# Performance work log

Hardware: AMD Instinct MI355X
Metric: run time of the kernel (lower is better)

## Reference

```python
import jax, jax.numpy as jnp
import numpy as np
from jax import lax

H = W = 16   # grid_size
C = 64       # d_model
NH = 4       # attention heads
DH = C // NH
L = 2        # transformer layers
FF = 2048    # torch TransformerEncoderLayer default dim_feedforward
B = 8192
FEAT = 55


def _feats(pi, pj, gi, gj, wall):
    # pi,pj,gi,gj: scalar int32; wall: [H,W] float32
    f = jnp.float32
    ain = 2.0 * pi.astype(f) / (H - 1) - 1.0
    ajn = 2.0 * pj.astype(f) / (W - 1) - 1.0
    gin = 2.0 * gi.astype(f) / (H - 1) - 1.0
    gjn = 2.0 * gj.astype(f) / (W - 1) - 1.0
    dxg = gjn - ajn
    dyg = gin - ain
    dg = jnp.sqrt(dxg * dxg + dyg * dyg + 1e-8)
    goal = jnp.stack([ain, ajn, gin, gjn, dxg, dyg, dg, dyg / dg, dxg / dg])
    # first (up to) 3 wall locations in row-major order
    flat = wall.reshape(-1)
    idx = jnp.arange(H * W, dtype=jnp.int32)
    masked = jnp.where(flat == 1, idx, H * W)
    top3 = -lax.top_k(-masked, 3)[0]            # 3 smallest flat indices
    is_valid = top3 < H * W
    valid = is_valid.astype(f)
    safe = jnp.where(is_valid, top3, 0)
    win = 2.0 * (safe // W).astype(f) / (H - 1) - 1.0   # [3]
    wjn = 2.0 * (safe % W).astype(f) / (W - 1) - 1.0

    def rel(rin, rjn):
        dx = wjn - rjn
        dy = win - rin
        d = jnp.sqrt(dx * dx + dy * dy + 1e-8)
        return jnp.stack([win, wjn, dx, dy, d, dy / d, dx / d], axis=1)  # [3,7]

    aw = (rel(ain, ajn) * valid[:, None]).reshape(21)
    gw = (rel(gin, gjn) * valid[:, None]).reshape(21)
    up = jnp.where(pi > 0, wall[jnp.clip(pi - 1, 0, H - 1), pj], 1.0)
    dn = jnp.where(pi < H - 1, wall[jnp.clip(pi + 1, 0, H - 1), pj], 1.0)
    lf = jnp.where(pj > 0, wall[pi, jnp.clip(pj - 1, 0, W - 1)], 1.0)
    rt = jnp.where(pj < W - 1, wall[pi, jnp.clip(pj + 1, 0, W - 1)], 1.0)
    neigh = jnp.stack([up, dn, lf, rt])
    return jnp.concatenate([goal, aw, gw, neigh])  # [55]


def _ln(x, g, b):
    m = x.mean(-1, keepdims=True)
    v = ((x - m) ** 2).mean(-1, keepdims=True)
    return (x - m) / jnp.sqrt(v + 1e-5) * g + b


def _mha(x, wqkv, bqkv, wo, bo):
    # x: [B,T,C]
    qkv = x @ wqkv.T + bqkv               # [B,T,3C]
    q, k, v = jnp.split(qkv, 3, axis=-1)
    hds = lambda t: t.reshape(t.shape[0], t.shape[1], NH, DH).transpose(0, 2, 1, 3)
    q, k, v = hds(q), hds(k), hds(v)
    a = jax.nn.softmax(jnp.einsum('bhqd,bhkd->bhqk', q, k) / np.sqrt(DH).astype(np.float32), axis=-1)
    o = jnp.einsum('bhqk,bhkd->bhqd', a, v).transpose(0, 2, 1, 3).reshape(x.shape)
    return o @ wo.T + bo


def _forward(ai, aj, gi, gj, walls,
             mlp_w1, mlp_b1, mlp_w2, mlp_b2,
             in_proj_w, in_proj_b, out_w, out_b,
             ln1_g, ln1_b, ln2_g, ln2_b,
             ffn_w1, ffn_b1, ffn_w2, ffn_b2):
    wf = walls.astype(jnp.float32)
    # 5 positions per obs: current + 4 hypothetical moves (stay in place if off-grid)
    moves = jnp.array([[0, 0], [-1, 0], [1, 0], [0, -1], [0, 1]], dtype=jnp.int32)
    ni = ai[:, None] + moves[None, :, 0]
    nj = aj[:, None] + moves[None, :, 1]
    inb = (ni >= 0) & (ni < H) & (nj >= 0) & (nj < W)
    pi = jnp.where(inb, ni, ai[:, None])   # [B,5]
    pj = jnp.where(inb, nj, aj[:, None])
    per_obs = jax.vmap(_feats, in_axes=(0, 0, None, None, None))
    feats = jax.vmap(per_obs, in_axes=(0, 0, 0, 0, 0))(pi, pj, gi, gj, wf)  # [B,5,55]
    # feat_mlp: Linear -> GELU(exact) -> Linear
    tok = jax.nn.gelu(feats @ mlp_w1.T + mlp_b1, approximate=False) @ mlp_w2.T + mlp_b2  # [B,5,C]
    x = tok
    for l in range(L):
        x = _ln(x + _mha(x, in_proj_w[l], in_proj_b[l], out_w[l], out_b[l]), ln1_g[l], ln1_b[l])
        hdn = jax.nn.relu(x @ ffn_w1[l].T + ffn_b1[l]) @ ffn_w2[l].T + ffn_b2[l]
        x = _ln(x + hdn, ln2_g[l], ln2_b[l])
    return x  # [B,5,C]


def setup_inputs() -> dict:
    key = jax.random.key(0)
    ks = jax.random.split(key, 24)
    s = 0.02
    inp = {
        'ai': jax.random.randint(ks[0], (B,), 0, H, dtype=jnp.int32),
        'aj': jax.random.randint(ks[1], (B,), 0, W, dtype=jnp.int32),
        'gi': jax.random.randint(ks[2], (B,), 0, H, dtype=jnp.int32),
        'gj': jax.random.randint(ks[3], (B,), 0, W, dtype=jnp.int32),
        'walls': jax.random.randint(ks[4], (B, H, W), 0, 2, dtype=jnp.int32),
        'mlp_w1': jax.random.normal(ks[5], (128, FEAT)) * s,
        'mlp_b1': jnp.zeros((128,)),
        'mlp_w2': jax.random.normal(ks[6], (C, 128)) * s,
        'mlp_b2': jnp.zeros((C,)),
        'in_proj_w': jax.random.normal(ks[7], (L, 3 * C, C)) * s,
        'in_proj_b': jnp.zeros((L, 3 * C)),
        'out_w': jax.random.normal(ks[8], (L, C, C)) * s,
        'out_b': jnp.zeros((L, C)),
        'ln1_g': jnp.ones((L, C)),
        'ln1_b': jnp.zeros((L, C)),
        'ln2_g': jnp.ones((L, C)),
        'ln2_b': jnp.zeros((L, C)),
        'ffn_w1': jax.random.normal(ks[9], (L, FF, C)) * s,
        'ffn_b1': jnp.zeros((L, FF)),
        'ffn_w2': jax.random.normal(ks[10], (L, C, FF)) * s,
        'ffn_b2': jnp.zeros((L, C)),
    }
    return inp


def reference(ai, aj, gi, gj, walls,
              mlp_w1, mlp_b1, mlp_w2, mlp_b2,
              in_proj_w, in_proj_b, out_w, out_b,
              ln1_g, ln1_b, ln2_g, ln2_b,
              ffn_w1, ffn_b1, ffn_w2, ffn_b2):
    return _forward(ai, aj, gi, gj, walls,
                    mlp_w1, mlp_b1, mlp_w2, mlp_b2,
                    in_proj_w, in_proj_b, out_w, out_b,
                    ln1_g, ln1_b, ln2_g, ln2_b,
                    ffn_w1, ffn_b1, ffn_w2, ffn_b2)
```

## Files before the change

### kernel.cpp

```cpp
#include <hip/hip_runtime.h>
#include <math.h>

#define NT 256

typedef __attribute__((ext_vector_type(4))) float  f32x4;
typedef __attribute__((ext_vector_type(8))) short  bf16x8;
typedef __attribute__((ext_vector_type(4))) short  bf16x4;

static __device__ __forceinline__ short f2bf(float f) {
    unsigned u = __builtin_bit_cast(unsigned, f);
    unsigned r = (u + 0x7fffu + ((u >> 16) & 1u)) >> 16;
    return (short)r;
}

static __device__ __forceinline__ unsigned pk2(float a, float b) {
    unsigned ua = __builtin_bit_cast(unsigned, a);
    unsigned ub = __builtin_bit_cast(unsigned, b);
    ua = (ua + 0x7fffu + ((ua >> 16) & 1u)) >> 16;
    ub = (ub + 0x7fffu + ((ub >> 16) & 1u)) & 0xffff0000u;
    return ua | ub;
}
static __device__ __forceinline__ bf16x4 pk_bf16(f32x4 d) {
    uint2 t;
    t.x = pk2(d[0], d[1]);
    t.y = pk2(d[2], d[3]);
    return __builtin_bit_cast(bf16x4, t);
}
static __device__ __forceinline__ bf16x8 pk_bf16x8(f32x4 a, f32x4 b) {
    uint4 t;
    t.x = pk2(a[0], a[1]);
    t.y = pk2(a[2], a[3]);
    t.z = pk2(b[0], b[1]);
    t.w = pk2(b[2], b[3]);
    return __builtin_bit_cast(bf16x8, t);
}
static __device__ __forceinline__ bf16x4 lo4(bf16x8 v) {
    return __builtin_shufflevector(v, v, 0, 1, 2, 3);
}
static __device__ __forceinline__ bf16x4 hi4(bf16x8 v) {
    return __builtin_shufflevector(v, v, 4, 5, 6, 7);
}

#define MFMA16x32(a, b, c) __builtin_amdgcn_mfma_f32_16x16x32_bf16(a, b, c, 0, 0, 0)

#if __has_builtin(__builtin_amdgcn_mfma_f32_16x16x16bf16_1k)
static __device__ __forceinline__ f32x4 mfma16x16(bf16x4 a, bf16x4 b, f32x4 c) {
    return __builtin_amdgcn_mfma_f32_16x16x16bf16_1k(a, b, c, 0, 0, 0);
}
#elif __has_builtin(__builtin_amdgcn_mfma_f32_16x16x16_bf16)
static __device__ __forceinline__ f32x4 mfma16x16(bf16x4 a, bf16x4 b, f32x4 c) {
    return __builtin_amdgcn_mfma_f32_16x16x16_bf16(a, b, c, 0, 0, 0);
}
#else
static __device__ __forceinline__ f32x4 mfma16x16(bf16x4 a, bf16x4 b, f32x4 c) {
    f32x4 d;
    asm("v_mfma_f32_16x16x16_bf16 %0, %1, %2, %3" : "=v"(d) : "v"(a), "v"(b), "v"(c));
    return d;
}
#endif

#define WS_FPK  0
#define WS_QKV  524288
#define WS_WO   548864
#define WS_BASE 557056
#define WS_MW1  557056
#define WS_MW2  565248
#define WS_TOTAL 573440

__global__ __launch_bounds__(NT) void k_cvtw(
    const float* __restrict__ ffn_w1, const float* __restrict__ ffn_w2,
    const float* __restrict__ in_proj_w, const float* __restrict__ out_w,
    const float* __restrict__ mlp_w1, const float* __restrict__ mlp_w2,
    int do_mlp,
    unsigned short* __restrict__ ws)
{
    int i = blockIdx.x * NT + threadIdx.x;
    if (i < 524288) {
        int l = i >> 18;
        int w = i & 262143;
        int c = w >> 13;
        int ww = w & 8191;
        int region = ww >> 11;
        int q = ww & 2047;
        int lane = q >> 3, j = q & 7;
        int hc = lane >> 6, lg = (lane >> 4) & 3, lr = lane & 15;
        const float* W1 = ffn_w1 + l * 131072;
        const float* W2 = ffn_w2 + l * 131072;
        float v;
        if (region == 0)
            v = W1[(c * 64 + hc * 16 + lr) * 64 + lg * 8 + j];
        else if (region == 1)
            v = W1[(c * 64 + hc * 16 + lr) * 64 + 32 + lg * 8 + j];
        else {
            int nf = ((region - 2) << 1) + (j >> 2);
            int r = j & 3;
            v = W2[(nf * 16 + lr) * 2048 + c * 64 + hc * 16 + lg * 4 + r];
        }
        ws[WS_FPK + i] = (unsigned short)f2bf(v);
    }
    if (i < 24576) ws[WS_QKV + i] = (unsigned short)f2bf(in_proj_w[i]);
    if (i < 8192)  ws[WS_WO + i]  = (unsigned short)f2bf(out_w[i]);
    if (do_mlp && i < 8192) {
        int row = i >> 6, col = i & 63;
        ws[WS_MW1 + i] = (col < 55) ? (unsigned short)f2bf(mlp_w1[row * 55 + col]) : 0;
        ws[WS_MW2 + i] = (unsigned short)f2bf(mlp_w2[i]);
    }
}

#define FB 16
__global__ __launch_bounds__(320) void k_feat2(
    const int* __restrict__ ai, const int* __restrict__ aj,
    const int* __restrict__ gi, const int* __restrict__ gj,
    const int* __restrict__ walls,
    const unsigned short* __restrict__ w1p,
    const float* __restrict__ b1,
    const unsigned short* __restrict__ w2p,
    const float* __restrict__ b2,
    float* __restrict__ x)
{
    const int tid = threadIdx.x;
    const int ob0 = blockIdx.x * FB;
    __shared__ unsigned char wl[FB * 256];
    __shared__ short fe[80][72];
    __shared__ int t3s[FB][3];

    for (int i = tid; i < FB * 256; i += 320)
        wl[i] = (unsigned char)walls[ob0 * 256 + i];
    __syncthreads();

    const int lane = tid & 63;
    const int wid  = tid >> 6;

    if (wid < 4) {
        #pragma unroll
        for (int q = 0; q < 4; ++q) {
            const int o = wid * 4 + q;
            const unsigned char* wp = wl + o * 256 + lane * 4;
            int m = (wp[0] ? 1 : 0) | (wp[1] ? 2 : 0) | (wp[2] ? 4 : 0) | (wp[3] ? 8 : 0);
            unsigned long long bm[4];
            bm[0] = __ballot(m & 1); bm[1] = __ballot(m & 2);
            bm[2] = __ballot(m & 4); bm[3] = __ballot(m & 8);
            int res[3];
            #pragma unroll
            for (int c = 0; c < 3; ++c) {
                int best = 1 << 30, bj = -1;
                #pragma unroll
                for (int j = 0; j < 4; ++j)
                    if (bm[j]) {
                        int cand = 4 * (int)__builtin_ctzll(bm[j]) + j;
                        if (cand < best) { best = cand; bj = j; }
                    }
                res[c] = (bj >= 0) ? best : 256;
                if (bj >= 0) bm[bj] &= bm[bj] - 1;
            }
            if (lane == 0) {
                t3s[o][0] = res[0]; t3s[o][1] = res[1]; t3s[o][2] = res[2];
            }
        }
    }
    __syncthreads();

    if (tid < 80) {
        const int o = tid / 5, tq = tid % 5;
        const int gob = ob0 + o;
        const unsigned char* wp = wl + o * 256;
        const int mi[5] = {0, -1, 1, 0, 0};
        const int mj[5] = {0, 0, 0, -1, 1};
        const int a_i = ai[gob], a_j = aj[gob];
        int ni = a_i + mi[tq], nj = a_j + mj[tq];
        bool inb = (ni >= 0 && ni < 16 && nj >= 0 && nj < 16);
        int pi = inb ? ni : a_i;
        int pj = inb ? nj : a_j;

        float f[64];
        #pragma unroll
        for (int d = 55; d < 64; ++d) f[d] = 0.f;

        const float ain = 2.f * (float)pi / 15.f - 1.f;
        const float ajn = 2.f * (float)pj / 15.f - 1.f;
        const float gin = 2.f * (float)gi[gob] / 15.f - 1.f;
        const float gjn = 2.f * (float)gj[gob] / 15.f - 1.f;
        const float dxg = gjn - ajn, dyg = gin - ain;
        const float dg = sqrtf(dxg * dxg + dyg * dyg + 1e-8f);
        f[0] = ain; f[1] = ajn; f[2] = gin; f[3] = gjn;
        f[4] = dxg; f[5] = dyg; f[6] = dg; f[7] = dyg / dg; f[8] = dxg / dg;

        #pragma unroll
        for (int w = 0; w < 3; ++w) {
            int idx = t3s[o][w];
            float vm = (idx < 256) ? 1.f : 0.f;
            int safe = (idx < 256) ? idx : 0;
            float win = 2.f * (float)(safe >> 4) / 15.f - 1.f;
            float wjn = 2.f * (float)(safe & 15) / 15.f - 1.f;
            {
                float dx = wjn - ajn, dy = win - ain;
                float d = sqrtf(dx * dx + dy * dy + 1e-8f);
                f[9 + w * 7 + 0] = win * vm; f[9 + w * 7 + 1] = wjn * vm;
                f[9 + w * 7 + 2] = dx * vm;  f[9 + w * 7 + 3] = dy * vm;
                f[9 + w * 7 + 4] = d * vm;
                f[9 + w * 7 + 5] = (dy / d) * vm; f[9 + w * 7 + 6] = (dx / d) * vm;
            }
            {
                float dx = wjn - gjn, dy = win - gin;
                float d = sqrtf(dx * dx + dy * dy + 1e-8f);
                f[30 + w * 7 + 0] = win * vm; f[30 + w * 7 + 1] = wjn * vm;
                f[30 + w * 7 + 2] = dx * vm;  f[30 + w * 7 + 3] = dy * vm;
                f[30 + w * 7 + 4] = d * vm;
                f[30 + w * 7 + 5] = (dy / d) * vm; f[30 + w * 7 + 6] = (dx / d) * vm;
            }
        }
        f[51] = (pi > 0)  ? (float)wp[(pi - 1) * 16 + pj] : 1.f;
        f[52] = (pi < 15) ? (float)wp[(pi + 1) * 16 + pj] : 1.f;
        f[53] = (pj > 0)  ? (float)wp[pi * 16 + (pj - 1)] : 1.f;
        f[54] = (pj < 15) ? (float)wp[pi * 16 + (pj + 1)] : 1.f;

        unsigned* dst = (unsigned*)&fe[tid][0];
        #pragma unroll
        for (int d = 0; d < 32; ++d)
            dst[d] = pk2(f[2 * d], f[2 * d + 1]);
    }
    __syncthreads();

    const int lr = lane & 15;
    const int lg = lane >> 4;
    const int t0 = wid * 16;

    bf16x8 bf0 = *(const bf16x8*)&fe[t0 + lr][lg * 8];
    bf16x8 bf1 = *(const bf16x8*)&fe[t0 + lr][32 + lg * 8];

    f32x4 acc[4] = {};
    #pragma unroll
    for (int hc = 0; hc < 8; ++hc) {
        bf16x8 a0 = *(const bf16x8*)(w1p + (hc * 16 + lr) * 64 + lg * 8);
        bf16x8 a1 = *(const bf16x8*)(w1p + (hc * 16 + lr) * 64 + 32 + lg * 8);
        f32x4 d = {0.f, 0.f, 0.f, 0.f};
        d = MFMA16x32(a0, bf0, d);
        d = MFMA16x32(a1, bf1, d);
        f32x4 b1v = *(const f32x4*)(b1 + hc * 16 + lg * 4);
        bf16x4 h;
        #pragma unroll
        for (int r = 0; r < 4; ++r) {
            float s = d[r] + b1v[r];
            h[r] = f2bf(0.5f * s * (1.f + erff(s * 0.70710678118654752f)));
        }
        #pragma unroll
        for (int nf = 0; nf < 4; ++nf) {
            bf16x4 bw = *(const bf16x4*)(w2p + (nf * 16 + lr) * 128 + hc * 16 + lg * 4);
            acc[nf] = mfma16x16(h, bw, acc[nf]);
        }
    }

    const int gt0 = blockIdx.x * 80 + t0;
    #pragma unroll
    for (int r = 0; r < 4; ++r) {
        const int row = (gt0 + lg * 4 + r) * 64;
        #pragma unroll
        for (int nf = 0; nf < 4; ++nf)
            x[row + nf * 16 + lr] = acc[nf][r] + b2[nf * 16 + lr];
    }
}

__global__ __launch_bounds__(NT) void k_feat(
    const int* __restrict__ ai, const int* __restrict__ aj,
    const int* __restrict__ gi, const int* __restrict__ gj,
    const int* __restrict__ walls,
    const float* __restrict__ w1, const float* __restrict__ b1,
    const float* __restrict__ w2, const float* __restrict__ b2,
    float* __restrict__ xout)
{
    const int b = blockIdx.x;
    const int tid = threadIdx.x;
    __shared__ float wallf[256];
    __shared__ unsigned long long wmask[4];
    __shared__ int   t3[3];
    __shared__ float feats[5][55];
    __shared__ float h1[5][128];

    int wv = walls[b * 256 + tid];
    wallf[tid] = (float)wv;
    unsigned long long bm = __ballot(wv == 1);
    if ((tid & 63) == 0) wmask[tid >> 6] = bm;
    __syncthreads();

    if (tid == 0) {
        int c = 0;
        for (int w = 0; w < 4 && c < 3; ++w) {
            unsigned long long mm = wmask[w];
            while (mm && c < 3) {
                t3[c++] = w * 64 + __builtin_ctzll(mm);
                mm &= mm - 1;
            }
        }
        for (; c < 3; ++c) t3[c] = 256;
    }
    __syncthreads();

    if (tid < 5) {
        const int mi[5] = {0, -1, 1, 0, 0};
        const int mj[5] = {0, 0, 0, -1, 1};
        const int a_i = ai[b], a_j = aj[b];
        int ni = a_i + mi[tid], nj = a_j + mj[tid];
        bool inb = (ni >= 0 && ni < 16 && nj >= 0 && nj < 16);
        int pi = inb ? ni : a_i;
        int pj = inb ? nj : a_j;

        const float ain = 2.f * (float)pi / 15.f - 1.f;
        const float ajn = 2.f * (float)pj / 15.f - 1.f;
        const float gin = 2.f * (float)gi[b] / 15.f - 1.f;
        const float gjn = 2.f * (float)gj[b] / 15.f - 1.f;
        const float dxg = gjn - ajn, dyg = gin - ain;
        const float dg = sqrtf(dxg * dxg + dyg * dyg + 1e-8f);

        float* f = feats[tid];
        f[0] = ain; f[1] = ajn; f[2] = gin; f[3] = gjn;
        f[4] = dxg; f[5] = dyg; f[6] = dg; f[7] = dyg / dg; f[8] = dxg / dg;

        for (int w = 0; w < 3; ++w) {
            int idx = t3[w];
            float vm = (idx < 256) ? 1.f : 0.f;
            int safe = (idx < 256) ? idx : 0;
            float win = 2.f * (float)(safe >> 4) / 15.f - 1.f;
            float wjn = 2.f * (float)(safe & 15) / 15.f - 1.f;
            {
                float dx = wjn - ajn, dy = win - ain;
                float d = sqrtf(dx * dx + dy * dy + 1e-8f);
                float* o = f + 9 + w * 7;
                o[0] = win * vm; o[1] = wjn * vm; o[2] = dx * vm; o[3] = dy * vm;
                o[4] = d * vm;  o[5] = (dy / d) * vm; o[6] = (dx / d) * vm;
            }
            {
                float dx = wjn - gjn, dy = win - gin;
                float d = sqrtf(dx * dx + dy * dy + 1e-8f);
                float* o = f + 30 + w * 7;
                o[0] = win * vm; o[1] = wjn * vm; o[2] = dx * vm; o[3] = dy * vm;
                o[4] = d * vm;  o[5] = (dy / d) * vm; o[6] = (dx / d) * vm;
            }
        }
        f[51] = (pi > 0)  ? wallf[(pi - 1) * 16 + pj] : 1.f;
        f[52] = (pi < 15) ? wallf[(pi + 1) * 16 + pj] : 1.f;
        f[53] = (pj > 0)  ? wallf[pi * 16 + (pj - 1)] : 1.f;
        f[54] = (pj < 15) ? wallf[pi * 16 + (pj + 1)] : 1.f;
    }
    __syncthreads();

    for (int i = tid; i < 640; i += NT) {
        int p = i >> 7, j = i & 127;
        float s = b1[j];
        const float* wr = w1 + j * 55;
        const float* fp = feats[p];
        #pragma unroll
        for (int k = 0; k < 55; ++k) s += fp[k] * wr[k];
        h1[p][j] = 0.5f * s * (1.f + erff(s * 0.70710678118654752f));
    }
    __syncthreads();

    for (int i = tid; i < 320; i += NT) {
        int p = i >> 6, j = i & 63;
        float s = b2[j];
        const float* wr = w2 + j * 128;
        #pragma unroll
        for (int k = 0; k < 128; ++k) s += h1[p][k] * wr[k];
        xout[b * 320 + i] = s;
    }
}

__global__ __launch_bounds__(256, 2) void k_att3(
    const float* __restrict__ x, float* __restrict__ xo,
    const unsigned short* __restrict__ wqkv,
    const float* __restrict__ bqkv,
    const unsigned short* __restrict__ wo,
    const float* __restrict__ bo,
    const float* __restrict__ g1, const float* __restrict__ be1)
{
    const int tid  = threadIdx.x;
    const int lane = tid & 63;
    const int wid  = tid >> 6;
    const int lr = lane & 15;
    const int lg = lane >> 4;
    const int o0 = blockIdx.x * 16;

    __shared__ unsigned short o_sh[5][16][68];
    __shared__ float          y_sh[5][16][68];

    bf16x8 bx[5][2];
    #pragma unroll
    for (int tq = 0; tq < 5; ++tq)
        #pragma unroll
        for (int kf = 0; kf < 2; ++kf) {
            const float* p = x + ((o0 + lr) * 5 + tq) * 64 + kf * 32 + lg * 8;
            f32x4 aa = *(const f32x4*)(p);
            f32x4 bb = *(const f32x4*)(p + 4);
            bx[tq][kf] = pk_bf16x8(aa, bb);
        }

    {
        const int h = wid;
        bf16x8 aq[2], ak[2], av[2];
        #pragma unroll
        for (int kf = 0; kf < 2; ++kf) {
            aq[kf] = *(const bf16x8*)(wqkv + (h * 16 + lr) * 64 + kf * 32 + lg * 8);
            ak[kf] = *(const bf16x8*)(wqkv + (64 + h * 16 + lr) * 64 + kf * 32 + lg * 8);
            av[kf] = *(const bf16x8*)(wqkv + (128 + h * 16 + lr) * 64 + kf * 32 + lg * 8);
        }
        f32x4 bq = *(const f32x4*)(bqkv + h * 16 + lg * 4);
        f32x4 bk = *(const f32x4*)(bqkv + 64 + h * 16 + lg * 4);
        f32x4 bv = *(const f32x4*)(bqkv + 128 + h * 16 + lg * 4);

        f32x4 qf[5], kf_[5], vf[5];
        #pragma unroll
        for (int t = 0; t < 5; ++t) {
            f32x4 d = {0.f, 0.f, 0.f, 0.f};
            d = MFMA16x32(aq[0], bx[t][0], d);
            d = MFMA16x32(aq[1], bx[t][1], d);
            qf[t] = d + bq;
            f32x4 e = {0.f, 0.f, 0.f, 0.f};
            e = MFMA16x32(ak[0], bx[t][0], e);
            e = MFMA16x32(ak[1], bx[t][1], e);
            kf_[t] = e + bk;
            f32x4 g = {0.f, 0.f, 0.f, 0.f};
            g = MFMA16x32(av[0], bx[t][0], g);
            g = MFMA16x32(av[1], bx[t][1], g);
            vf[t] = g + bv;
        }

        float p_[5][5];
        #pragma unroll
        for (int tq = 0; tq < 5; ++tq)
            #pragma unroll
            for (int tk = 0; tk < 5; ++tk) {
                float s = qf[tq][0] * kf_[tk][0] + qf[tq][1] * kf_[tk][1]
                        + qf[tq][2] * kf_[tk][2] + qf[tq][3] * kf_[tk][3];
                s += __shfl_xor(s, 16);
                s += __shfl_xor(s, 32);
                p_[tq][tk] = s * 0.25f;
            }
        #pragma unroll
        for (int tq = 0; tq < 5; ++tq) {
            float m = p_[tq][0];
            #pragma unroll
            for (int tk = 1; tk < 5; ++tk) m = fmaxf(m, p_[tq][tk]);
            float sum = 0.f;
            #pragma unroll
            for (int tk = 0; tk < 5; ++tk) {
                float e = __expf(p_[tq][tk] - m);
                p_[tq][tk] = e; sum += e;
            }
            float inv = 1.f / sum;
            #pragma unroll
            for (int tk = 0; tk < 5; ++tk) p_[tq][tk] *= inv;
        }

        #pragma unroll
        for (int tq = 0; tq < 5; ++tq) {
            f32x4 o = {0.f, 0.f, 0.f, 0.f};
            #pragma unroll
            for (int tk = 0; tk < 5; ++tk) o += p_[tq][tk] * vf[tk];
            *(bf16x4*)&o_sh[tq][lr][h * 16 + lg * 4] = pk_bf16(o);
        }
    }
    __syncthreads();

    {
        bf16x4 bwo[4];
        #pragma unroll
        for (int kf = 0; kf < 4; ++kf)
            bwo[kf] = *(const bf16x4*)(wo + (wid * 16 + lr) * 64 + kf * 16 + lg * 4);

        #pragma unroll
        for (int tq = 0; tq < 5; ++tq) {
            f32x4 acc = {0.f, 0.f, 0.f, 0.f};
            #pragma unroll
            for (int kf = 0; kf < 4; ++kf) {
                bf16x4 a2 = *(const bf16x4*)&o_sh[tq][lr][kf * 16 + lg * 4];
                acc = mfma16x16(a2, bwo[kf], acc);
            }
            const int col = wid * 16 + lr;
            const float bv2 = bo[col];
            #pragma unroll
            for (int r = 0; r < 4; ++r) {
                const int obs = lg * 4 + r;
                y_sh[tq][obs][col] =
                    acc[r] + bv2 + x[((o0 + obs) * 5 + tq) * 64 + col];
            }
        }
    }
    __syncthreads();

    {
        const int grp = tid >> 4;
        const int l16 = tid & 15;
        #pragma unroll
        for (int it = 0; it < 5; ++it) {
            const int tq = it, obs = grp;
            f32x4 v = *(const f32x4*)&y_sh[tq][obs][l16 * 4];
            float s = v[0] + v[1] + v[2] + v[3];
            s += __shfl_xor(s, 1); s += __shfl_xor(s, 2);
            s += __shfl_xor(s, 4); s += __shfl_xor(s, 8);
            float mean = s * (1.f / 64.f);
            float q = 0.f;
            #pragma unroll
            for (int j = 0; j < 4; ++j) { float d0 = v[j] - mean; q += d0 * d0; }
            q += __shfl_xor(q, 1); q += __shfl_xor(q, 2);
            q += __shfl_xor(q, 4); q += __shfl_xor(q, 8);
            float rstd = rsqrtf(q * (1.f / 64.f) + 1e-5f);
            const int row = ((o0 + obs) * 5 + tq) * 64;
            #pragma unroll
            for (int j = 0; j < 4; ++j) {
                int c = l16 * 4 + j;
                xo[row + c] = (v[j] - mean) * rstd * g1[c] + be1[c];
            }
        }
    }
}

__global__ __launch_bounds__(NT) void k_att(
    float* __restrict__ x,
    const float* __restrict__ wqkv, const float* __restrict__ bqkv,
    const float* __restrict__ wo, const float* __restrict__ bo,
    const float* __restrict__ g1, const float* __restrict__ be1)
{
    const int b = blockIdx.x;
    const int tid = threadIdx.x;
    __shared__ float xs[5][64];
    __shared__ float qkv[5][192];
    __shared__ float att[4][5][5];
    __shared__ float os[5][64];
    __shared__ float xr[5][64];
    __shared__ float stat[5][2];

    for (int i = tid; i < 320; i += NT) xs[i >> 6][i & 63] = x[b * 320 + i];
    __syncthreads();

    for (int i = tid; i < 960; i += NT) {
        int p = i / 192, j = i % 192;
        float s = bqkv[j];
        const float* wr = wqkv + j * 64;
        const float* xm = xs[p];
        #pragma unroll
        for (int k = 0; k < 64; ++k) s += xm[k] * wr[k];
        qkv[p][j] = s;
    }
    __syncthreads();

    if (tid < 100) {
        int h = tid / 25, r = tid % 25, q = r / 5, kk = r % 5;
        float s = 0.f;
        #pragma unroll
        for (int d = 0; d < 16; ++d) s += qkv[q][h * 16 + d] * qkv[kk][64 + h * 16 + d];
        att[h][q][kk] = s * 0.25f;
    }
    __syncthreads();

    if (tid < 20) {
        int h = tid / 5, q = tid % 5;
        float m = att[h][q][0];
        for (int k = 1; k < 5; ++k) m = fmaxf(m, att[h][q][k]);
        float sum = 0.f;
        for (int k = 0; k < 5; ++k) { float e = expf(att[h][q][k] - m); att[h][q][k] = e; sum += e; }
        float inv = 1.f / sum;
        for (int k = 0; k < 5; ++k) att[h][q][k] *= inv;
    }
    __syncthreads();

    for (int i = tid; i < 320; i += NT) {
        int p = i >> 6, c = i & 63, h = c >> 4;
        float s = 0.f;
        #pragma unroll
        for (int k = 0; k < 5; ++k) s += att[h][p][k] * qkv[k][128 + c];
        os[p][c] = s;
    }
    __syncthreads();

    for (int i = tid; i < 320; i += NT) {
        int p = i >> 6, c = i & 63;
        float s = bo[c];
        const float* wr = wo + c * 64;
        const float* om = os[p];
        #pragma unroll
        for (int k = 0; k < 64; ++k) s += om[k] * wr[k];
        xr[p][c] = xs[p][c] + s;
    }
    __syncthreads();

    if (tid < 5) {
        float m = 0.f;
        for (int k = 0; k < 64; ++k) m += xr[tid][k];
        m *= (1.f / 64.f);
        float v = 0.f;
        for (int k = 0; k < 64; ++k) { float d = xr[tid][k] - m; v += d * d; }
        v *= (1.f / 64.f);
        stat[tid][0] = m;
        stat[tid][1] = 1.f / sqrtf(v + 1e-5f);
    }
    __syncthreads();

    for (int i = tid; i < 320; i += NT) {
        int p = i >> 6, c = i & 63;
        x[b * 320 + i] = (xr[p][c] - stat[p][0]) * stat[p][1] * g1[c] + be1[c];
    }
}

#define PKCH 8192
__global__ __launch_bounds__(256, 2) void k_ffn8(
    float* __restrict__ x,
    const unsigned short* __restrict__ wpk,
    const float* __restrict__ b1,
    const float* __restrict__ b2,
    const float* __restrict__ g2, const float* __restrict__ be2)
{
    __shared__ float red[4][4][4][64][4];
    const int tid  = threadIdx.x;
    const int lane = tid & 63;
    const int wid  = tid >> 6;
    const int lr = lane & 15;
    const int lg = lane >> 4;
    const int row0 = blockIdx.x * 64;

    bf16x8 bx[4][2];
    #pragma unroll
    for (int mf = 0; mf < 4; ++mf)
        #pragma unroll
        for (int kk = 0; kk < 2; ++kk) {
            const float* p = x + (row0 + mf * 16 + lr) * 64 + kk * 32 + lg * 8;
            f32x4 aa = *(const f32x4*)(p);
            f32x4 bb = *(const f32x4*)(p + 4);
            bx[mf][kk] = pk_bf16x8(aa, bb);
        }

    f32x4 acc[4][4] = {};
    const int fbase = (lg * 16 + lr) * 8;
    const unsigned short* wp = wpk + (wid * 8) * PKCH;
    const float* b1w = b1 + wid * 512;

    for (int c = 0; c < 8; ++c) {
        const unsigned short* L = wp + c * PKCH;
        bf16x8 rA[4], rB[4], rC[4], rD[4];
        #pragma unroll
        for (int hc = 0; hc < 4; ++hc) {
            rA[hc] = *(const bf16x8*)&L[hc * 512 + fbase];
            rB[hc] = *(const bf16x8*)&L[2048 + hc * 512 + fbase];
            rC[hc] = *(const bf16x8*)&L[4096 + hc * 512 + fbase];
            rD[hc] = *(const bf16x8*)&L[6144 + hc * 512 + fbase];
        }
        f32x4 b1v[4];
        #pragma unroll
        for (int hc = 0; hc < 4; ++hc)
            b1v[hc] = *(const f32x4*)(b1w + c * 64 + hc * 16 + lg * 4);

        #pragma unroll
        for (int hc = 0; hc < 4; ++hc) {
            #pragma unroll
            for (int mf = 0; mf < 4; ++mf) {
                f32x4 d = MFMA16x32(rA[hc], bx[mf][0], b1v[hc]);
                d = MFMA16x32(rB[hc], bx[mf][1], d);
                #pragma unroll
                for (int r = 0; r < 4; ++r) d[r] = fmaxf(d[r], 0.f);
                bf16x4 h = pk_bf16(d);
                acc[mf][0] = mfma16x16(h, lo4(rC[hc]), acc[mf][0]);
                acc[mf][1] = mfma16x16(h, hi4(rC[hc]), acc[mf][1]);
                acc[mf][2] = mfma16x16(h, lo4(rD[hc]), acc[mf][2]);
                acc[mf][3] = mfma16x16(h, hi4(rD[hc]), acc[mf][3]);
            }
        }
    }

    #pragma unroll
    for (int mf = 0; mf < 4; ++mf)
        #pragma unroll
        for (int nf = 0; nf < 4; ++nf)
            *(f32x4*)&red[wid][mf][nf][lane][0] = acc[mf][nf];
    __syncthreads();

    f32x4 vr[4];
    #pragma unroll
    for (int nf = 0; nf < 4; ++nf) {
        f32x4 s0 = *(const f32x4*)&red[0][wid][nf][lane][0];
        f32x4 s1 = *(const f32x4*)&red[1][wid][nf][lane][0];
        f32x4 s2 = *(const f32x4*)&red[2][wid][nf][lane][0];
        f32x4 s3 = *(const f32x4*)&red[3][wid][nf][lane][0];
        vr[nf] = (s0 + s1) + (s2 + s3);
    }

    #pragma unroll
    for (int r = 0; r < 4; ++r) {
        const int m = row0 + wid * 16 + lg * 4 + r;
        float v[4];
        float s = 0.f;
        #pragma unroll
        for (int nf = 0; nf < 4; ++nf) {
            int cc = nf * 16 + lr;
            float y = vr[nf][r] + b2[cc] + x[m * 64 + cc];
            v[nf] = y; s += y;
        }
        s += __shfl_xor(s, 1); s += __shfl_xor(s, 2);
        s += __shfl_xor(s, 4); s += __shfl_xor(s, 8);
        float mean = s * (1.f / 64.f);
        float q = 0.f;
        #pragma unroll
        for (int nf = 0; nf < 4; ++nf) { float d0 = v[nf] - mean; q += d0 * d0; }
        q += __shfl_xor(q, 1); q += __shfl_xor(q, 2);
        q += __shfl_xor(q, 4); q += __shfl_xor(q, 8);
        float rstd = rsqrtf(q * (1.f / 64.f) + 1e-5f);
        #pragma unroll
        for (int nf = 0; nf < 4; ++nf) {
            int cc = nf * 16 + lr;
            x[m * 64 + cc] = (v[nf] - mean) * rstd * g2[cc] + be2[cc];
        }
    }
}

#define GRP 8
#define ROWS (GRP * 5)
__global__ __launch_bounds__(NT) void k_ffn(
    float* __restrict__ x,
    const float* __restrict__ w1, const float* __restrict__ b1,
    const float* __restrict__ w2, const float* __restrict__ b2,
    const float* __restrict__ g2, const float* __restrict__ be2)
{
    const int tid = threadIdx.x;
    const int base = blockIdx.x * (ROWS * 64);
    __shared__ float xs[ROWS][64];
    __shared__ float hch[ROWS][128];
    __shared__ float stat[ROWS][2];

    for (int i = tid; i < ROWS * 64; i += NT) xs[i >> 6][i & 63] = x[base + i];
    __syncthreads();

    const int c = tid & 63;
    const int g = tid >> 6;
    float acc[10];
    #pragma unroll
    for (int r = 0; r < 10; ++r) acc[r] = 0.f;

    for (int ch = 0; ch < 16; ++ch) {
        for (int ii = tid; ii < ROWS * 128; ii += NT) {
            int m = ii >> 7, j = ii & 127;
            int jj = (ch << 7) + j;
            float s = b1[jj];
            const float* wr = w1 + jj * 64;
            const float* xm = xs[m];
            #pragma unroll
            for (int k = 0; k < 64; ++k) s += xm[k] * wr[k];
            hch[m][j] = fmaxf(s, 0.f);
        }
        __syncthreads();
        const float* w2r = w2 + c * 2048 + (ch << 7);
        for (int j = 0; j < 128; ++j) {
            float wv = w2r[j];
            #pragma unroll
            for (int r = 0; r < 10; ++r) acc[r] += hch[g * 10 + r][j] * wv;
        }
        __syncthreads();
    }

    #pragma unroll
    for (int r = 0; r < 10; ++r) {
        int m = g * 10 + r;
        hch[m][c] = acc[r] + b2[c] + xs[m][c];
    }
    __syncthreads();

    if (tid < ROWS) {
        float m = 0.f;
        for (int k = 0; k < 64; ++k) m += hch[tid][k];
        m *= (1.f / 64.f);
        float v = 0.f;
        for (int k = 0; k < 64; ++k) { float d = hch[tid][k] - m; v += d * d; }
        v *= (1.f / 64.f);
        stat[tid][0] = m;
        stat[tid][1] = 1.f / sqrtf(v + 1e-5f);
    }
    __syncthreads();

    for (int i = tid; i < ROWS * 64; i += NT) {
        int m = i >> 6, cc = i & 63;
        x[base + i] = (hch[m][cc] - stat[m][0]) * stat[m][1] * g2[cc] + be2[cc];
    }
}

extern "C" void kernel_launch(void* const* d_in, const int* in_sizes, int n_in,
                              void* d_out, int out_size, void* d_ws, size_t ws_size,
                              hipStream_t stream)
{
    (void)in_sizes; (void)n_in; (void)out_size;
    const int*   ai       = (const int*)d_in[0];
    const int*   aj       = (const int*)d_in[1];
    const int*   gi       = (const int*)d_in[2];
    const int*   gj       = (const int*)d_in[3];
    const int*   walls    = (const int*)d_in[4];
    const float* mlp_w1   = (const float*)d_in[5];
    const float* mlp_b1   = (const float*)d_in[6];
    const float* mlp_w2   = (const float*)d_in[7];
    const float* mlp_b2   = (const float*)d_in[8];
    const float* in_proj_w = (const float*)d_in[9];
    const float* in_proj_b = (const float*)d_in[10];
    const float* out_w    = (const float*)d_in[11];
    const float* out_b    = (const float*)d_in[12];
    const float* ln1_g    = (const float*)d_in[13];
    const float* ln1_b    = (const float*)d_in[14];
    const float* ln2_g    = (const float*)d_in[15];
    const float* ln2_b    = (const float*)d_in[16];
    const float* ffn_w1   = (const float*)d_in[17];
    const float* ffn_b1   = (const float*)d_in[18];
    const float* ffn_w2   = (const float*)d_in[19];
    const float* ffn_b2   = (const float*)d_in[20];

    float* x = (float*)d_out;
    const int B = 8192;
    const bool fast  = ws_size >= (size_t)(WS_BASE * 2);
    const bool fast2 = ws_size >= (size_t)(WS_TOTAL * 2);
    unsigned short* wsbf = (unsigned short*)d_ws;

    if (fast)
        k_cvtw<<<2048, NT, 0, stream>>>(ffn_w1, ffn_w2, in_proj_w, out_w,
                                        mlp_w1, mlp_w2, fast2 ? 1 : 0, wsbf);

    if (fast2) {
        k_feat2<<<B / FB, 320, 0, stream>>>(ai, aj, gi, gj, walls,
            wsbf + WS_MW1, mlp_b1, wsbf + WS_MW2, mlp_b2, x);
    } else {
        k_feat<<<B, NT, 0, stream>>>(ai, aj, gi, gj, walls,
                                     mlp_w1, mlp_b1, mlp_w2, mlp_b2, x);
    }

    for (int l = 0; l < 2; ++l) {
        if (fast) {
            k_att3<<<512, 256, 0, stream>>>(x, x,
                wsbf + WS_QKV + l * 12288, in_proj_b + l * 192,
                wsbf + WS_WO + l * 4096, out_b + l * 64,
                ln1_g + l * 64, ln1_b + l * 64);
            k_ffn8<<<640, 256, 0, stream>>>(x,
                wsbf + WS_FPK + l * 262144, ffn_b1 + l * 2048,
                ffn_b2 + l * 64,
                ln2_g + l * 64, ln2_b + l * 64);
        } else {
            k_att<<<B, NT, 0, stream>>>(x,
                in_proj_w + l * 192 * 64, in_proj_b + l * 192,
                out_w + l * 64 * 64, out_b + l * 64,
                ln1_g + l * 64, ln1_b + l * 64);
            k_ffn<<<B / GRP, NT, 0, stream>>>(x,
                ffn_w1 + l * 2048 * 64, ffn_b1 + l * 2048,
                ffn_w2 + l * 64 * 2048, ffn_b2 + l * 64,
                ln2_g + l * 64, ln2_b + l * 64);
        }
    }
}
```

Before: 149.1 us.

## Use 16x16x32 MFMA for FFN down-projection and shrink LDS reduction buffer

Repacks the W2 weights so that two adjacent hidden chunks are concatenated into one 8-wide bf16 operand. Each pair of 16x16x16 MFMAs in the second FFN GEMM becomes a single 16x16x32 MFMA, halving the MFMA instruction count there. The cross-wave reduction buffer is cut to a quarter by reducing one 16-row group at a time, with two barriers per group. The occupancy hint is raised from 2 to 3 blocks per CU, which risks register pressure or spills in exchange for more waves and less shared memory per block.

```diff
diff --git a/kernel.cpp b/kernel.cpp
--- a/kernel.cpp
+++ b/kernel.cpp
@@ -34,11 +34,8 @@
     t.w = pk2(b[2], b[3]);
     return __builtin_bit_cast(bf16x8, t);
 }
-static __device__ __forceinline__ bf16x4 lo4(bf16x8 v) {
-    return __builtin_shufflevector(v, v, 0, 1, 2, 3);
-}
-static __device__ __forceinline__ bf16x4 hi4(bf16x8 v) {
-    return __builtin_shufflevector(v, v, 4, 5, 6, 7);
+static __device__ __forceinline__ bf16x8 cat44(bf16x4 a, bf16x4 b) {
+    return __builtin_shufflevector(a, b, 0, 1, 2, 3, 4, 5, 6, 7);
 }
 
 #define MFMA16x32(a, b, c) __builtin_amdgcn_mfma_f32_16x16x32_bf16(a, b, c, 0, 0, 0)
@@ -82,19 +79,23 @@
         int ww = w & 8191;
         int region = ww >> 11;
         int q = ww & 2047;
-        int lane = q >> 3, j = q & 7;
-        int hc = lane >> 6, lg = (lane >> 4) & 3, lr = lane & 15;
         const float* W1 = ffn_w1 + l * 131072;
         const float* W2 = ffn_w2 + l * 131072;
         float v;
-        if (region == 0)
-            v = W1[(c * 64 + hc * 16 + lr) * 64 + lg * 8 + j];
-        else if (region == 1)
-            v = W1[(c * 64 + hc * 16 + lr) * 64 + 32 + lg * 8 + j];
-        else {
-            int nf = ((region - 2) << 1) + (j >> 2);
-            int r = j & 3;
-            v = W2[(nf * 16 + lr) * 2048 + c * 64 + hc * 16 + lg * 4 + r];
+        if (region <= 1) {
+            int lane = q >> 3, j = q & 7;
+            int lg = (lane >> 4) & 3, lr = lane & 15;
+            int hc = lane >> 6;
+            v = W1[(c * 64 + hc * 16 + lr) * 64 + region * 32 + lg * 8 + j];
+        } else {
+            int sub = q >> 9;
+            int rem = q & 511;
+            int lane16 = rem >> 3, j = rem & 7;
+            int lg = lane16 >> 4, lr = lane16 & 15;
+            int P = sub >> 1, nfh = sub & 1;
+            int nf = (region - 2) * 2 + nfh;
+            int ell = P * 32 + ((j >> 2) << 4) + lg * 4 + (j & 3);
+            v = W2[(nf * 16 + lr) * 2048 + c * 64 + ell];
         }
         ws[WS_FPK + i] = (unsigned short)f2bf(v);
     }
@@ -601,14 +602,14 @@
 }
 
 #define PKCH 8192
-__global__ __launch_bounds__(256, 2) void k_ffn8(
+__global__ __launch_bounds__(256, 3) void k_ffn9(
     float* __restrict__ x,
     const unsigned short* __restrict__ wpk,
     const float* __restrict__ b1,
     const float* __restrict__ b2,
     const float* __restrict__ g2, const float* __restrict__ be2)
 {
-    __shared__ float red[4][4][4][64][4];
+    __shared__ float red[4][4][64][4];
     const int tid  = threadIdx.x;
     const int lane = tid & 63;
     const int wid  = tid >> 6;
@@ -634,78 +635,88 @@
 
     for (int c = 0; c < 8; ++c) {
         const unsigned short* L = wp + c * PKCH;
-        bf16x8 rA[4], rB[4], rC[4], rD[4];
+        bf16x8 rA[4], rB[4], rW[2][4];
         #pragma unroll
         for (int hc = 0; hc < 4; ++hc) {
             rA[hc] = *(const bf16x8*)&L[hc * 512 + fbase];
             rB[hc] = *(const bf16x8*)&L[2048 + hc * 512 + fbase];
-            rC[hc] = *(const bf16x8*)&L[4096 + hc * 512 + fbase];
-            rD[hc] = *(const bf16x8*)&L[6144 + hc * 512 + fbase];
-        }
+        }
+        #pragma unroll
+        for (int P = 0; P < 2; ++P)
+            #pragma unroll
+            for (int nf = 0; nf < 4; ++nf)
+                rW[P][nf] = *(const bf16x8*)
+                    &L[4096 + (nf >> 1) * 2048 + (P * 2 + (nf & 1)) * 512 + fbase];
         f32x4 b1v[4];
         #pragma unroll
         for (int hc = 0; hc < 4; ++hc)
             b1v[hc] = *(const f32x4*)(b1w + c * 64 + hc * 16 + lg * 4);
 
         #pragma unroll
-        for (int hc = 0; hc < 4; ++hc) {
-            #pragma unroll
-            for (int mf = 0; mf < 4; ++mf) {
+        for (int mf = 0; mf < 4; ++mf) {
+            bf16x4 h[4];
+            #pragma unroll
+            for (int hc = 0; hc < 4; ++hc) {
                 f32x4 d = MFMA16x32(rA[hc], bx[mf][0], b1v[hc]);
                 d = MFMA16x32(rB[hc], bx[mf][1], d);
                 #pragma unroll
                 for (int r = 0; r < 4; ++r) d[r] = fmaxf(d[r], 0.f);
-                bf16x4 h = pk_bf16(d);
-                acc[mf][0] = mfma16x16(h, lo4(rC[hc]), acc[mf][0]);
-                acc[mf][1] = mfma16x16(h, hi4(rC[hc]), acc[mf][1]);
-                acc[mf][2] = mfma16x16(h, lo4(rD[hc]), acc[mf][2]);
-                acc[mf][3] = mfma16x16(h, hi4(rD[hc]), acc[mf][3]);
-            }
-        }
-    }
-
-    #pragma unroll
-    for (int mf = 0; mf < 4; ++mf)
+                h[hc] = pk_bf16(d);
+            }
+            #pragma unroll
+            for (int P = 0; P < 2; ++P) {
+                bf16x8 hp = cat44(h[2 * P], h[2 * P + 1]);
+                acc[mf][0] = MFMA16x32(hp, rW[P][0], acc[mf][0]);
+                acc[mf][1] = MFMA16x32(hp, rW[P][1], acc[mf][1]);
+                acc[mf][2] = MFMA16x32(hp, rW[P][2], acc[mf][2]);
+                acc[mf][3] = MFMA16x32(hp, rW[P][3], acc[mf][3]);
+            }
+        }
+    }
+
+    for (int m = 0; m < 4; ++m) {
         #pragma unroll
         for (int nf = 0; nf < 4; ++nf)
-            *(f32x4*)&red[wid][mf][nf][lane][0] = acc[mf][nf];
-    __syncthreads();
-
-    f32x4 vr[4];
-    #pragma unroll
-    for (int nf = 0; nf < 4; ++nf) {
-        f32x4 s0 = *(const f32x4*)&red[0][wid][nf][lane][0];
-        f32x4 s1 = *(const f32x4*)&red[1][wid][nf][lane][0];
-        f32x4 s2 = *(const f32x4*)&red[2][wid][nf][lane][0];
-        f32x4 s3 = *(const f32x4*)&red[3][wid][nf][lane][0];
-        vr[nf] = (s0 + s1) + (s2 + s3);
-    }
-
-    #pragma unroll
-    for (int r = 0; r < 4; ++r) {
-        const int m = row0 + wid * 16 + lg * 4 + r;
-        float v[4];
-        float s = 0.f;
-        #pragma unroll
-        for (int nf = 0; nf < 4; ++nf) {
-            int cc = nf * 16 + lr;
-            float y = vr[nf][r] + b2[cc] + x[m * 64 + cc];
-            v[nf] = y; s += y;
-        }
-        s += __shfl_xor(s, 1); s += __shfl_xor(s, 2);
-        s += __shfl_xor(s, 4); s += __shfl_xor(s, 8);
-        float mean = s * (1.f / 64.f);
-        float q = 0.f;
-        #pragma unroll
-        for (int nf = 0; nf < 4; ++nf) { float d0 = v[nf] - mean; q += d0 * d0; }
-        q += __shfl_xor(q, 1); q += __shfl_xor(q, 2);
-        q += __shfl_xor(q, 4); q += __shfl_xor(q, 8);
-        float rstd = rsqrtf(q * (1.f / 64.f) + 1e-5f);
-        #pragma unroll
-        for (int nf = 0; nf < 4; ++nf) {
-            int cc = nf * 16 + lr;
-            x[m * 64 + cc] = (v[nf] - mean) * rstd * g2[cc] + be2[cc];
-        }
+            *(f32x4*)&red[wid][nf][lane][0] = acc[m][nf];
+        __syncthreads();
+        if (wid == m) {
+            f32x4 vr[4];
+            #pragma unroll
+            for (int nf = 0; nf < 4; ++nf) {
+                f32x4 s0 = *(const f32x4*)&red[0][nf][lane][0];
+                f32x4 s1 = *(const f32x4*)&red[1][nf][lane][0];
+                f32x4 s2 = *(const f32x4*)&red[2][nf][lane][0];
+                f32x4 s3 = *(const f32x4*)&red[3][nf][lane][0];
+                vr[nf] = (s0 + s1) + (s2 + s3);
+            }
+            #pragma unroll
+            for (int r = 0; r < 4; ++r) {
+                const int mm = row0 + m * 16 + lg * 4 + r;
+                float v[4];
+                float s = 0.f;
+                #pragma unroll
+                for (int nf = 0; nf < 4; ++nf) {
+                    int cc = nf * 16 + lr;
+                    float y = vr[nf][r] + b2[cc] + x[mm * 64 + cc];
+                    v[nf] = y; s += y;
+                }
+                s += __shfl_xor(s, 1); s += __shfl_xor(s, 2);
+                s += __shfl_xor(s, 4); s += __shfl_xor(s, 8);
+                float mean = s * (1.f / 64.f);
+                float q = 0.f;
+                #pragma unroll
+                for (int nf = 0; nf < 4; ++nf) { float d0 = v[nf] - mean; q += d0 * d0; }
+                q += __shfl_xor(q, 1); q += __shfl_xor(q, 2);
+                q += __shfl_xor(q, 4); q += __shfl_xor(q, 8);
+                float rstd = rsqrtf(q * (1.f / 64.f) + 1e-5f);
+                #pragma unroll
+                for (int nf = 0; nf < 4; ++nf) {
+                    int cc = nf * 16 + lr;
+                    x[mm * 64 + cc] = (v[nf] - mean) * rstd * g2[cc] + be2[cc];
+                }
+            }
+        }
+        __syncthreads();
     }
 }
 
@@ -829,7 +840,7 @@
                 wsbf + WS_QKV + l * 12288, in_proj_b + l * 192,
                 wsbf + WS_WO + l * 4096, out_b + l * 64,
                 ln1_g + l * 64, ln1_b + l * 64);
-            k_ffn8<<<640, 256, 0, stream>>>(x,
+            k_ffn9<<<640, 256, 0, stream>>>(x,
                 wsbf + WS_FPK + l * 262144, ffn_b1 + l * 2048,
                 ffn_b2 + l * 64,
                 ln2_g + l * 64, ln2_b + l * 64);
```

After: 153.0 us. 2.6% more time.
